# Kernel optimization log

Hardware: AMD Instinct MI355X
Metric: run time of the kernel (lower is better)

Reference implementation:

```python
import jax, jax.numpy as jnp
import numpy as np

OUTLINER_RATIO_1 = 0.01
OUTLINER_RATIO_2 = 0.01


def get_statistics(x, outliner_ratio):
    # threshold such that ~outliner_ratio fraction of entries (by magnitude) are outliers
    return jnp.quantile(jnp.abs(x), 1.0 - outliner_ratio)


def outlier_svd_compress(x, thresh, rank):
    # split into sparse outlier part + low-rank factorization of the residual
    x_out = jnp.where(jnp.abs(x) > thresh, x, jnp.zeros((), x.dtype))  # outlier part
    x_sub = x - x_out                                                   # sub-outlier residual
    d = x.shape[-1]
    x2d = x_sub.reshape(-1, d)                                          # (B*H*S, D)
    _, _, vt = jnp.linalg.svd(x2d, full_matrices=False)                 # economy SVD
    R = vt[:rank].T                                                     # (D, rank)
    L = x2d @ R                                                         # (B*H*S, rank)
    return x_out, L, R


def setup_inputs() -> dict:
    key = jax.random.key(0)
    k1, k2 = jax.random.split(key)
    x1 = jax.random.normal(k1, (2, 16, 2048, 128), dtype=jnp.float32)
    x2 = jax.random.normal(k2, (2, 16, 128, 2048), dtype=jnp.float32)
    return {"x1": x1, "x2": x2, "rank": 16}


def reference(x1, x2, rank):
    # forward result (iteration 0: statistics + SVD compression are computed,
    # but only the GEMM result is the module's forward output)
    result = jnp.einsum("bhsd,bhdt->bhst", x1, x2)
    # compression pipeline executed each step (saved-for-backward side effects)
    t1 = get_statistics(x1, OUTLINER_RATIO_1)
    t2 = get_statistics(jnp.swapaxes(x2, -2, -1), OUTLINER_RATIO_2)
    _ = outlier_svd_compress(x1, t1, rank)
    _ = outlier_svd_compress(jnp.swapaxes(x2, -2, -1), t2, rank)
    return result
```

## Files before the change

### kernel.cpp

```cpp
#include <hip/hip_runtime.h>
#include <hip/hip_bf16.h>

typedef __attribute__((ext_vector_type(8))) short bf16x8;
typedef __attribute__((ext_vector_type(4))) float f32x4;

__device__ __forceinline__ unsigned short f2bf(float f) {
    unsigned int u = __builtin_bit_cast(unsigned int, f);
    u += 0x7fffu + ((u >> 16) & 1u);
    return (unsigned short)(u >> 16);
}

__device__ __forceinline__ int swz(int r, int k ) {
    int unit = k >> 3;
    return r * 256 + (((unit ^ (r & 15)) << 4) | ((k & 7) << 1));
}

#define LDS_B_OFF 32768

__global__ __launch_bounds__(256, 2)
void gemm_bf16_batched(const float* __restrict__ A,
                       const float* __restrict__ B,
                       float* __restrict__ C) {
    __shared__ __align__(16) unsigned char lds[65536];

    const int bid = blockIdx.x;
    const int bh = bid >> 8;
    const int mt = (bid >> 4) & 15;
    const int nt = bid & 15;

    const float* Ag = A + (size_t)bh * (2048 * 128) + (size_t)mt * (128 * 128);
    const float* Bg = B + (size_t)bh * (128 * 2048) + nt * 128;
    float*       Cg = C + (size_t)bh * (2048 * 2048) + (size_t)(mt * 128) * 2048 + nt * 128;

    const int t = threadIdx.x;

#pragma unroll
    for (int i = 0; i < 16; ++i) {
        const int e = i * 1024 + t * 4;
        const int m = e >> 7;
        const int k = e & 127;
        const float4 v = *(const float4*)(Ag + m * 128 + k);
        uint2 w;
        w.x = (unsigned int)f2bf(v.x) | ((unsigned int)f2bf(v.y) << 16);
        w.y = (unsigned int)f2bf(v.z) | ((unsigned int)f2bf(v.w) << 16);
        *(uint2*)(&lds[swz(m, k)]) = w;
    }

#pragma unroll
    for (int s = 0; s < 4; ++s) {
        const int k0 = s * 32 + ((t >> 5) << 2);
        const int n0 = (t & 31) << 2;
        const float4 r0 = *(const float4*)(Bg + (size_t)(k0 + 0) * 2048 + n0);
        const float4 r1 = *(const float4*)(Bg + (size_t)(k0 + 1) * 2048 + n0);
        const float4 r2 = *(const float4*)(Bg + (size_t)(k0 + 2) * 2048 + n0);
        const float4 r3 = *(const float4*)(Bg + (size_t)(k0 + 3) * 2048 + n0);
        const float c0[4] = {r0.x, r0.y, r0.z, r0.w};
        const float c1[4] = {r1.x, r1.y, r1.z, r1.w};
        const float c2[4] = {r2.x, r2.y, r2.z, r2.w};
        const float c3[4] = {r3.x, r3.y, r3.z, r3.w};
#pragma unroll
        for (int j = 0; j < 4; ++j) {
            uint2 w;
            w.x = (unsigned int)f2bf(c0[j]) | ((unsigned int)f2bf(c1[j]) << 16);
            w.y = (unsigned int)f2bf(c2[j]) | ((unsigned int)f2bf(c3[j]) << 16);
            *(uint2*)(&lds[LDS_B_OFF + swz(n0 + j, k0)]) = w;
        }
    }

    __syncthreads();

    const int l  = t & 63;
    const int w  = t >> 6;
    const int wm = (w >> 1) * 64;
    const int wn = (w & 1) * 64;
    const int lr = l & 15;
    const int lg = l >> 4;

    f32x4 acc[4][4] = {};

#pragma unroll
    for (int kk = 0; kk < 4; ++kk) {
        const int kbase = kk * 32 + lg * 8;
        bf16x8 a[4], b[4];
#pragma unroll
        for (int mi = 0; mi < 4; ++mi)
            a[mi] = *(const bf16x8*)(&lds[swz(wm + mi * 16 + lr, kbase)]);
#pragma unroll
        for (int ni = 0; ni < 4; ++ni)
            b[ni] = *(const bf16x8*)(&lds[LDS_B_OFF + swz(wn + ni * 16 + lr, kbase)]);
#pragma unroll
        for (int mi = 0; mi < 4; ++mi)
#pragma unroll
            for (int ni = 0; ni < 4; ++ni)
                acc[mi][ni] = __builtin_amdgcn_mfma_f32_16x16x32_bf16(
                    a[mi], b[ni], acc[mi][ni], 0, 0, 0);
    }

#pragma unroll
    for (int mi = 0; mi < 4; ++mi) {
#pragma unroll
        for (int ni = 0; ni < 4; ++ni) {
            const int row = wm + mi * 16 + lg * 4;
            const int col = wn + ni * 16 + lr;
#pragma unroll
            for (int j = 0; j < 4; ++j) {
                __builtin_nontemporal_store(acc[mi][ni][j],
                                            Cg + (size_t)(row + j) * 2048 + col);
            }
        }
    }
}

extern "C" void kernel_launch(void* const* d_in, const int* in_sizes, int n_in,
                              void* d_out, int out_size, void* d_ws, size_t ws_size,
                              hipStream_t stream) {
    const float* x1 = (const float*)d_in[0];
    const float* x2 = (const float*)d_in[1];
    float* out = (float*)d_out;
    gemm_bf16_batched<<<dim3(8192), dim3(256), 0, stream>>>(x1, x2, out);
}
```

Before: 175.3 us.

## Load A fragments directly from global into registers, halve LDS footprint

A operand tiles are no longer staged through shared memory. Each wave now reads its A fragments straight from global memory and converts them to bf16 in registers inside the k-loop. That halves LDS use to 32KB and raises launch bounds to 4 blocks per SM to increase occupancy. The trade is redundant global and L2 reads of A, since the two column waves share the same rows, plus a non-unrolled k-loop with exposed load latency.

```diff
diff --git a/kernel.cpp b/kernel.cpp
--- a/kernel.cpp
+++ b/kernel.cpp
@@ -15,13 +15,11 @@
     return r * 256 + (((unit ^ (r & 15)) << 4) | ((k & 7) << 1));
 }
 
-#define LDS_B_OFF 32768
-
-__global__ __launch_bounds__(256, 2)
+__global__ __launch_bounds__(256, 4)
 void gemm_bf16_batched(const float* __restrict__ A,
                        const float* __restrict__ B,
                        float* __restrict__ C) {
-    __shared__ __align__(16) unsigned char lds[65536];
+    __shared__ __align__(16) unsigned char lds[32768];
 
     const int bid = blockIdx.x;
     const int bh = bid >> 8;
@@ -33,18 +31,6 @@
     float*       Cg = C + (size_t)bh * (2048 * 2048) + (size_t)(mt * 128) * 2048 + nt * 128;
 
     const int t = threadIdx.x;
-
-#pragma unroll
-    for (int i = 0; i < 16; ++i) {
-        const int e = i * 1024 + t * 4;
-        const int m = e >> 7;
-        const int k = e & 127;
-        const float4 v = *(const float4*)(Ag + m * 128 + k);
-        uint2 w;
-        w.x = (unsigned int)f2bf(v.x) | ((unsigned int)f2bf(v.y) << 16);
-        w.y = (unsigned int)f2bf(v.z) | ((unsigned int)f2bf(v.w) << 16);
-        *(uint2*)(&lds[swz(m, k)]) = w;
-    }
 
 #pragma unroll
     for (int s = 0; s < 4; ++s) {
@@ -63,7 +49,7 @@
             uint2 w;
             w.x = (unsigned int)f2bf(c0[j]) | ((unsigned int)f2bf(c1[j]) << 16);
             w.y = (unsigned int)f2bf(c2[j]) | ((unsigned int)f2bf(c3[j]) << 16);
-            *(uint2*)(&lds[LDS_B_OFF + swz(n0 + j, k0)]) = w;
+            *(uint2*)(&lds[swz(n0 + j, k0)]) = w;
         }
     }
 
@@ -78,16 +64,29 @@
 
     f32x4 acc[4][4] = {};
 
-#pragma unroll
+#pragma unroll 1
     for (int kk = 0; kk < 4; ++kk) {
         const int kbase = kk * 32 + lg * 8;
-        bf16x8 a[4], b[4];
+
+        bf16x8 a[4];
 #pragma unroll
-        for (int mi = 0; mi < 4; ++mi)
-            a[mi] = *(const bf16x8*)(&lds[swz(wm + mi * 16 + lr, kbase)]);
+        for (int mi = 0; mi < 4; ++mi) {
+            const float* p = Ag + (size_t)(wm + mi * 16 + lr) * 128 + kbase;
+            const float4 lo = *(const float4*)(p);
+            const float4 hi = *(const float4*)(p + 4);
+            bf16x8 av;
+            av[0] = (short)f2bf(lo.x); av[1] = (short)f2bf(lo.y);
+            av[2] = (short)f2bf(lo.z); av[3] = (short)f2bf(lo.w);
+            av[4] = (short)f2bf(hi.x); av[5] = (short)f2bf(hi.y);
+            av[6] = (short)f2bf(hi.z); av[7] = (short)f2bf(hi.w);
+            a[mi] = av;
+        }
+
+        bf16x8 b[4];
 #pragma unroll
         for (int ni = 0; ni < 4; ++ni)
-            b[ni] = *(const bf16x8*)(&lds[LDS_B_OFF + swz(wn + ni * 16 + lr, kbase)]);
+            b[ni] = *(const bf16x8*)(&lds[swz(wn + ni * 16 + lr, kbase)]);
+
 #pragma unroll
         for (int mi = 0; mi < 4; ++mi)
 #pragma unroll
```

Result: slower. 179.5 us (+2.4%).
